# Optimization experiments

Measured on AMD Instinct MI355X. Metric: run time of the kernel, lower is better.

The kernel has to match this reference:

```python
import jax, jax.numpy as jnp
import numpy as np

N_NODES = 50000
N_EDGES = 800000
IN_CH = 16
OUT_CH = 16
HID = 32


def setup_inputs() -> dict:
    key = jax.random.key(0)
    ks = jax.random.split(key, 10)
    features = jax.random.normal(ks[0], (N_NODES, IN_CH), dtype=jnp.float32)
    coords = jax.random.normal(ks[1], (N_NODES, 3), dtype=jnp.float32)
    # edges without self-loops (avoids zero-distance edges)
    row = jax.random.randint(ks[2], (N_EDGES,), 0, N_NODES, dtype=jnp.int32)
    off = jax.random.randint(ks[3], (N_EDGES,), 1, N_NODES, dtype=jnp.int32)
    col = (row + off) % N_NODES
    edge_index = jnp.stack([row, col], axis=0)
    # params (fan-in scaled like torch defaults, roughly)
    w1 = jax.random.normal(ks[4], (1, HID), dtype=jnp.float32)
    b1 = jnp.zeros((HID,), dtype=jnp.float32)
    w2 = jax.random.normal(ks[5], (HID, HID), dtype=jnp.float32) / np.sqrt(HID)
    b2 = jnp.zeros((HID,), dtype=jnp.float32)
    wc = jax.random.normal(ks[6], (HID, IN_CH * OUT_CH), dtype=jnp.float32) / np.sqrt(HID)
    bc = jnp.zeros((IN_CH * OUT_CH,), dtype=jnp.float32)
    return {"features": features, "coords": coords, "edge_index": edge_index,
            "w1": w1, "b1": b1, "w2": w2, "b2": b2, "wc": wc, "bc": bc}


def reference(features, coords, edge_index, w1, b1, w2, b2, wc, bc):
    row, col = edge_index[0], edge_index[1]
    rel_pos = coords[row] - coords[col]                      # [E, 3]
    distances = jnp.sqrt(jnp.sum(rel_pos * rel_pos, axis=-1, keepdims=True))  # [E, 1]
    h = jax.nn.silu(distances @ w1 + b1)                     # [E, H]
    h = jax.nn.silu(h @ w2 + b2)                             # [E, H]
    coeffs = (h @ wc + bc).reshape(-1, OUT_CH, IN_CH)        # [E, out, in]
    # Faithful to torch einsum 'noi,ei->no': the edge axes of coeffs and
    # neighbor_features are DISTINCT labels, so features[col] is summed over
    # all edges, then contracted with each edge's coeff matrix.
    feat_sum = jnp.sum(features[col], axis=0)                # [in]
    messages = jnp.einsum('eoi,i->eo', coeffs, feat_sum)     # [E, out]
    out = jnp.zeros((features.shape[0], OUT_CH), dtype=features.dtype)
    out = out.at[row].add(messages)                          # scatter-add
    return out
```

## Files before the change

kernel.cpp:

```cpp
#include <hip/hip_runtime.h>
#include <hip/hip_bf16.h>

#define IN_CH 16
#define OUT_CH 16
#define HID 32
#define NSLICE 8
#define SDEG 16
#define G_TAB 8192
#define DMAX 16.0f
#define R1_BLOCKS 64
#define TB 256

__device__ __forceinline__ float silu(float x) {
  return x * __frcp_rn(1.f + __expf(-x));
}

__global__ __launch_bounds__(256) void k_pass1(
    const float* __restrict__ feat, const float* __restrict__ coords,
    const int* __restrict__ row, const int* __restrict__ col, int E, int N,
    int* __restrict__ cnt8, float* __restrict__ bucket,
    float* __restrict__ partials) {
  int e = blockIdx.x * blockDim.x + threadIdx.x;
  int lane = threadIdx.x & 63;
  int wave = threadIdx.x >> 6;
  bool act = (e < E);

  float s[IN_CH];
#pragma unroll
  for (int i = 0; i < IN_CH; ++i) s[i] = 0.f;

  int r = 0, pos = SDEG;
  float d = 0.f;
  int slice = blockIdx.x & (NSLICE - 1);

  if (act) {
    r = row[e];
    int c = col[e];

    float rx = coords[r * 3 + 0] - coords[c * 3 + 0];
    float ry = coords[r * 3 + 1] - coords[c * 3 + 1];
    float rz = coords[r * 3 + 2] - coords[c * 3 + 2];
    d = sqrtf(rx * rx + ry * ry + rz * rz);

    pos = atomicAdd(&cnt8[r * NSLICE + slice], 1);

    const float4* fp = reinterpret_cast<const float4*>(feat + (size_t)c * IN_CH);
    float4 a = fp[0], b = fp[1], cc = fp[2], dd = fp[3];
    s[0] = a.x;  s[1] = a.y;  s[2] = a.z;  s[3] = a.w;
    s[4] = b.x;  s[5] = b.y;  s[6] = b.z;  s[7] = b.w;
    s[8] = cc.x; s[9] = cc.y; s[10] = cc.z; s[11] = cc.w;
    s[12] = dd.x; s[13] = dd.y; s[14] = dd.z; s[15] = dd.w;
  }

  __shared__ float red[4][IN_CH];
#pragma unroll
  for (int i = 0; i < IN_CH; ++i) {
    float v = s[i];
#pragma unroll
    for (int off = 32; off > 0; off >>= 1) v += __shfl_down(v, off);
    s[i] = v;
  }
  if (lane == 0) {
#pragma unroll
    for (int i = 0; i < IN_CH; ++i) red[wave][i] = s[i];
  }
  __syncthreads();
  if (threadIdx.x < IN_CH) {
    int i = threadIdx.x;
    partials[(size_t)blockIdx.x * IN_CH + i] =
        red[0][i] + red[1][i] + red[2][i] + red[3][i];
  }

  if (act && pos < SDEG)
    bucket[(size_t)r * (NSLICE * SDEG) + slice * SDEG + pos] = d;
}

__global__ __launch_bounds__(256) void k_reduce1(
    const float* __restrict__ partials, int nrows, float* __restrict__ stage2) {
  __shared__ float red[16][IN_CH];
  int t = threadIdx.x;
  int ch = t & 15, g = t >> 4;
  int stream_id = blockIdx.x * 16 + g;
  int stride = 16 * gridDim.x;
  float a = 0.f;
  for (int rr = stream_id; rr < nrows; rr += stride)
    a += partials[(size_t)rr * IN_CH + ch];
  red[g][ch] = a;
  __syncthreads();
  if (t < IN_CH) {
    float s = 0.f;
#pragma unroll
    for (int g2 = 0; g2 < 16; ++g2) s += red[g2][t];
    stage2[(size_t)blockIdx.x * IN_CH + t] = s;
  }
}

__global__ __launch_bounds__(512) void k_wce(
    const float* __restrict__ rows_in, int nrows,
    const float* __restrict__ wc, const float* __restrict__ bc,
    float* __restrict__ wce, float* __restrict__ bce) {
  __shared__ float seg[32][IN_CH];
  __shared__ float sfs[IN_CH];
  int t = threadIdx.x;
  {
    int ch = t & 15, sg = t >> 4;
    float a = 0.f;
    for (int rr = sg; rr < nrows; rr += 32)
      a += rows_in[(size_t)rr * IN_CH + ch];
    seg[sg][ch] = a;
  }
  __syncthreads();
  if (t < IN_CH) {
    float a = 0.f;
#pragma unroll
    for (int sg = 0; sg < 32; ++sg) a += seg[sg][t];
    sfs[t] = a;
  }
  __syncthreads();

  int k = t >> 4, o = t & 15;
  float acc = 0.f;
#pragma unroll
  for (int i = 0; i < IN_CH; ++i)
    acc += wc[k * (IN_CH * OUT_CH) + o * IN_CH + i] * sfs[i];
  wce[t] = acc;

  if (t < OUT_CH) {
    float a = 0.f;
#pragma unroll
    for (int i = 0; i < IN_CH; ++i) a += bc[t * IN_CH + i] * sfs[i];
    bce[t] = a;
  }
}

__global__ __launch_bounds__(TB) void k_table(
    const float* __restrict__ w1, const float* __restrict__ b1,
    const float* __restrict__ w2, const float* __restrict__ b2,
    const float* __restrict__ wce, const float* __restrict__ bce,
    float* __restrict__ tableP) {
  __shared__ float F[TB][OUT_CH];
  int base = blockIdx.x * (TB - 1);
  int i = base + threadIdx.x;

  float m[OUT_CH];
#pragma unroll
  for (int o = 0; o < OUT_CH; ++o) m[o] = 0.f;

  if (i < G_TAB) {
    float d = (float)i * (DMAX / (float)(G_TAB - 1));

    float h1[HID];
#pragma unroll
    for (int k = 0; k < HID; ++k) h1[k] = silu(d * w1[k] + b1[k]);

    float h2[HID];
#pragma unroll
    for (int k = 0; k < HID; ++k) h2[k] = b2[k];
#pragma unroll
    for (int k = 0; k < HID; ++k) {
      float hk = h1[k];
#pragma unroll
      for (int j = 0; j < HID; ++j) h2[j] += hk * w2[k * HID + j];
    }

#pragma unroll
    for (int o = 0; o < OUT_CH; ++o) m[o] = bce[o];
#pragma unroll
    for (int k = 0; k < HID; ++k) {
      float hk = silu(h2[k]);
#pragma unroll
      for (int o = 0; o < OUT_CH; ++o) m[o] += hk * wce[k * OUT_CH + o];
    }
  }

#pragma unroll
  for (int o = 0; o < OUT_CH; ++o) F[threadIdx.x][o] = m[o];
  __syncthreads();

  const int NV4 = (TB - 1) * OUT_CH * 2 / 4;
  for (int v = threadIdx.x; v < NV4; v += TB) {
    int flat = v * 4;
    int p = flat >> 5;
    int w = flat & 31;
    int c0 = w >> 1;
    int P = base + p;
    if (P < G_TAB - 1) {
      float4 val = make_float4(F[p][c0], F[p + 1][c0],
                               F[p][c0 + 1], F[p + 1][c0 + 1]);
      *reinterpret_cast<float4*>(tableP + ((size_t)P * OUT_CH + c0) * 2) = val;
    }
  }
}

__global__ __launch_bounds__(256) void k_gather_tab(
    const int* __restrict__ cnt8, const float* __restrict__ bucket, int N,
    const float* __restrict__ tableP, float* __restrict__ out) {
  int wave = threadIdx.x >> 6;
  int lane = threadIdx.x & 63;
  int n = blockIdx.x * 4 + wave;
  if (n >= N) return;

  int g = lane >> 4;
  int ch = lane & 15;

  const float2* bp =
      reinterpret_cast<const float2*>(bucket + (size_t)n * (NSLICE * SDEG));
  float2 d2 = bp[lane];

  int c8 = 0;
  if (lane < NSLICE) c8 = cnt8[n * NSLICE + lane];
  int cntA = min(__shfl(c8, g), SDEG);
  int cntB = min(__shfl(c8, g + 4), SDEG);

  int jmax = max(cntA, cntB);
#pragma unroll
  for (int off = 32; off > 0; off >>= 1)
    jmax = max(jmax, __shfl_xor(jmax, off));

  const float inv = (float)(G_TAB - 1) / DMAX;
  float acc = 0.f;
  for (int j = 0; j < jmax; ++j) {
    {
      int slot = g * SDEG + j;
      float dx = __shfl(d2.x, slot >> 1);
      float dy = __shfl(d2.y, slot >> 1);
      float d = (slot & 1) ? dy : dx;
      if (j < cntA) {
        float x = d * inv;
        int i0 = (int)x;
        i0 = min(i0, G_TAB - 2);
        float frac = x - (float)i0;
        float2 f = *reinterpret_cast<const float2*>(
            tableP + ((size_t)i0 * OUT_CH + ch) * 2);
        acc += f.x + frac * (f.y - f.x);
      }
    }
    {
      int slot = (g + 4) * SDEG + j;
      float dx = __shfl(d2.x, slot >> 1);
      float dy = __shfl(d2.y, slot >> 1);
      float d = (slot & 1) ? dy : dx;
      if (j < cntB) {
        float x = d * inv;
        int i0 = (int)x;
        i0 = min(i0, G_TAB - 2);
        float frac = x - (float)i0;
        float2 f = *reinterpret_cast<const float2*>(
            tableP + ((size_t)i0 * OUT_CH + ch) * 2);
        acc += f.x + frac * (f.y - f.x);
      }
    }
  }

  acc += __shfl_xor(acc, 16);
  acc += __shfl_xor(acc, 32);
  if (lane < OUT_CH) out[(size_t)n * OUT_CH + lane] = acc;
}

__global__ __launch_bounds__(256) void k_hist(
    const int* __restrict__ col, int E, int* __restrict__ ccnt) {
  int e = blockIdx.x * blockDim.x + threadIdx.x;
  if (e < E) atomicAdd(&ccnt[col[e]], 1);
}

__global__ __launch_bounds__(256) void k_fs(
    const float* __restrict__ feat, const int* __restrict__ ccnt, int N,
    float* __restrict__ partials) {
  int ch = threadIdx.x & 15;
  int slot = threadIdx.x >> 4;
  int gs = blockIdx.x * 16 + slot;
  int stride = 16 * gridDim.x;
  float a = 0.f;
  for (int n = gs; n < N; n += stride)
    a += (float)ccnt[n] * feat[(size_t)n * IN_CH + ch];
  __shared__ float red[16][IN_CH];
  red[slot][ch] = a;
  __syncthreads();
  if (threadIdx.x < IN_CH) {
    int i = threadIdx.x;
    float s = 0.f;
#pragma unroll
    for (int g = 0; g < 16; ++g) s += red[g][i];
    partials[(size_t)blockIdx.x * IN_CH + i] = s;
  }
}

__global__ __launch_bounds__(256) void k_edges_atomic(
    const float* __restrict__ coords, const int* __restrict__ row,
    const int* __restrict__ col, int E,
    const float* __restrict__ w1, const float* __restrict__ b1,
    const float* __restrict__ w2, const float* __restrict__ b2,
    const float* __restrict__ wce, const float* __restrict__ bce,
    float* __restrict__ out) {
  int e = blockIdx.x * blockDim.x + threadIdx.x;
  if (e >= E) return;
  int r = row[e], c = col[e];
  float rx = coords[r * 3 + 0] - coords[c * 3 + 0];
  float ry = coords[r * 3 + 1] - coords[c * 3 + 1];
  float rz = coords[r * 3 + 2] - coords[c * 3 + 2];
  float d = sqrtf(rx * rx + ry * ry + rz * rz);
  float h1[HID];
#pragma unroll
  for (int k = 0; k < HID; ++k) h1[k] = silu(d * w1[k] + b1[k]);
  float h2[HID];
#pragma unroll
  for (int k = 0; k < HID; ++k) h2[k] = b2[k];
#pragma unroll
  for (int k = 0; k < HID; ++k) {
    float hk = h1[k];
#pragma unroll
    for (int j = 0; j < HID; ++j) h2[j] += hk * w2[k * HID + j];
  }
  float m[OUT_CH];
#pragma unroll
  for (int o = 0; o < OUT_CH; ++o) m[o] = bce[o];
#pragma unroll
  for (int k = 0; k < HID; ++k) {
    float hk = silu(h2[k]);
#pragma unroll
    for (int o = 0; o < OUT_CH; ++o) m[o] += hk * wce[k * OUT_CH + o];
  }
  float* op = out + (size_t)r * OUT_CH;
#pragma unroll
  for (int o = 0; o < OUT_CH; ++o) atomicAdd(op + o, m[o]);
}

extern "C" void kernel_launch(void* const* d_in, const int* in_sizes, int n_in,
                              void* d_out, int out_size, void* d_ws,
                              size_t ws_size, hipStream_t stream) {
  const float* features = (const float*)d_in[0];
  const float* coords   = (const float*)d_in[1];
  const int*   eidx     = (const int*)d_in[2];
  const float* w1       = (const float*)d_in[3];
  const float* b1       = (const float*)d_in[4];
  const float* w2       = (const float*)d_in[5];
  const float* b2       = (const float*)d_in[6];
  const float* wc       = (const float*)d_in[7];
  const float* bc       = (const float*)d_in[8];

  const int E = in_sizes[2] / 2;
  const int N = in_sizes[0] / IN_CH;
  const int* row = eidx;
  const int* col = eidx + E;

  float* out = (float*)d_out;
  const int eb = (E + 255) / 256;

  float* wce      = (float*)d_ws;
  float* bce      = wce + 512;
  float* stage2   = bce + 16;
  float* partials = stage2 + R1_BLOCKS * IN_CH;
  float* tableP   = partials + (size_t)eb * IN_CH;
  int*   cnt8     = (int*)(tableP + (size_t)G_TAB * OUT_CH * 2);
  float* bucket   = (float*)(cnt8 + (size_t)N * NSLICE);

  size_t needed = (512 + 16 + (size_t)R1_BLOCKS * IN_CH + (size_t)eb * IN_CH +
                   (size_t)G_TAB * OUT_CH * 2) * 4 +
                  (size_t)N * NSLICE * 4 + (size_t)N * NSLICE * SDEG * 4;

  if (ws_size >= needed) {
    hipMemsetAsync(cnt8, 0, (size_t)N * NSLICE * sizeof(int), stream);
    k_pass1<<<eb, 256, 0, stream>>>(features, coords, row, col, E, N, cnt8,
                                    bucket, partials);
    k_reduce1<<<R1_BLOCKS, 256, 0, stream>>>(partials, eb, stage2);
    k_wce<<<1, 512, 0, stream>>>(stage2, R1_BLOCKS, wc, bc, wce, bce);
    int tb_grid = (G_TAB - 1 + (TB - 1) - 1) / (TB - 1) + 1;
    k_table<<<tb_grid, TB, 0, stream>>>(w1, b1, w2, b2, wce, bce, tableP);
    int gb = (N + 3) / 4;
    k_gather_tab<<<gb, 256, 0, stream>>>(cnt8, bucket, N, tableP, out);
  } else {
    float* partials_fb = bce + 16;
    int*   ccnt_fb     = (int*)(partials_fb + 64 * IN_CH);
    hipMemsetAsync(ccnt_fb, 0, (size_t)N * sizeof(int), stream);
    hipMemsetAsync(out, 0, (size_t)out_size * sizeof(float), stream);
    k_hist<<<eb, 256, 0, stream>>>(col, E, ccnt_fb);
    k_fs<<<64, 256, 0, stream>>>(features, ccnt_fb, N, partials_fb);
    k_wce<<<1, 512, 0, stream>>>(partials_fb, 64, wc, bc, wce, bce);
    k_edges_atomic<<<eb, 256, 0, stream>>>(coords, row, col, E, w1, b1, w2,
                                           b2, wce, bce, out);
  }
}
```

Before: 100.9 us.

## Compute feature sum via per-column histogram instead of per-edge feature gather

The first pass no longer gathers 64 bytes of features per edge and no longer does a block reduction. Instead it atomically counts column occurrences into sliced counters. A separate kernel then computes the feature sum as a count-weighted sum over nodes, which replaces the partials reduction kernel. The memset is also replaced by a custom zeroing kernel covering both counter arrays. This trades per-edge feature reads and shuffle reductions for an extra atomic per edge and an extra pass over the nodes. In the fallback path the zeroing kernel writes int4 chunks, so it can write up to 3 ints past the N-int counter array.

```diff
diff --git a/kernel.cpp b/kernel.cpp
--- a/kernel.cpp
+++ b/kernel.cpp
@@ -8,90 +8,62 @@
 #define SDEG 16
 #define G_TAB 8192
 #define DMAX 16.0f
-#define R1_BLOCKS 64
 #define TB 256
 
 __device__ __forceinline__ float silu(float x) {
   return x * __frcp_rn(1.f + __expf(-x));
 }
 
+__global__ __launch_bounds__(256) void k_zero(int4* __restrict__ p, int n4) {
+  int i = blockIdx.x * blockDim.x + threadIdx.x;
+  if (i < n4) p[i] = make_int4(0, 0, 0, 0);
+}
+
 __global__ __launch_bounds__(256) void k_pass1(
-    const float* __restrict__ feat, const float* __restrict__ coords,
-    const int* __restrict__ row, const int* __restrict__ col, int E, int N,
-    int* __restrict__ cnt8, float* __restrict__ bucket,
+    const float* __restrict__ coords, const int* __restrict__ row,
+    const int* __restrict__ col, int E,
+    int* __restrict__ cnt8, int* __restrict__ ccnt8,
+    float* __restrict__ bucket) {
+  int e = blockIdx.x * blockDim.x + threadIdx.x;
+  if (e >= E) return;
+  int slice = blockIdx.x & (NSLICE - 1);
+  int r = row[e], c = col[e];
+
+  atomicAdd(&ccnt8[c * NSLICE + slice], 1);
+
+  float rx = coords[r * 3 + 0] - coords[c * 3 + 0];
+  float ry = coords[r * 3 + 1] - coords[c * 3 + 1];
+  float rz = coords[r * 3 + 2] - coords[c * 3 + 2];
+  float d = sqrtf(rx * rx + ry * ry + rz * rz);
+
+  int pos = atomicAdd(&cnt8[r * NSLICE + slice], 1);
+  if (pos < SDEG)
+    bucket[(size_t)r * (NSLICE * SDEG) + slice * SDEG + pos] = d;
+}
+
+__global__ __launch_bounds__(256) void k_fs8(
+    const float* __restrict__ feat, const int* __restrict__ ccnt8, int N,
     float* __restrict__ partials) {
-  int e = blockIdx.x * blockDim.x + threadIdx.x;
-  int lane = threadIdx.x & 63;
-  int wave = threadIdx.x >> 6;
-  bool act = (e < E);
-
-  float s[IN_CH];
-#pragma unroll
-  for (int i = 0; i < IN_CH; ++i) s[i] = 0.f;
-
-  int r = 0, pos = SDEG;
-  float d = 0.f;
-  int slice = blockIdx.x & (NSLICE - 1);
-
-  if (act) {
-    r = row[e];
-    int c = col[e];
-
-    float rx = coords[r * 3 + 0] - coords[c * 3 + 0];
-    float ry = coords[r * 3 + 1] - coords[c * 3 + 1];
-    float rz = coords[r * 3 + 2] - coords[c * 3 + 2];
-    d = sqrtf(rx * rx + ry * ry + rz * rz);
-
-    pos = atomicAdd(&cnt8[r * NSLICE + slice], 1);
-
-    const float4* fp = reinterpret_cast<const float4*>(feat + (size_t)c * IN_CH);
-    float4 a = fp[0], b = fp[1], cc = fp[2], dd = fp[3];
-    s[0] = a.x;  s[1] = a.y;  s[2] = a.z;  s[3] = a.w;
-    s[4] = b.x;  s[5] = b.y;  s[6] = b.z;  s[7] = b.w;
-    s[8] = cc.x; s[9] = cc.y; s[10] = cc.z; s[11] = cc.w;
-    s[12] = dd.x; s[13] = dd.y; s[14] = dd.z; s[15] = dd.w;
-  }
-
-  __shared__ float red[4][IN_CH];
-#pragma unroll
-  for (int i = 0; i < IN_CH; ++i) {
-    float v = s[i];
-#pragma unroll
-    for (int off = 32; off > 0; off >>= 1) v += __shfl_down(v, off);
-    s[i] = v;
-  }
-  if (lane == 0) {
-#pragma unroll
-    for (int i = 0; i < IN_CH; ++i) red[wave][i] = s[i];
-  }
+  int ch = threadIdx.x & 15;
+  int slot = threadIdx.x >> 4;
+  int gs = blockIdx.x * 16 + slot;
+  int stride = 16 * gridDim.x;
+  float a = 0.f;
+  for (int n = gs; n < N; n += stride) {
+    const int4* cp = reinterpret_cast<const int4*>(ccnt8 + (size_t)n * NSLICE);
+    int4 c0 = cp[0], c1 = cp[1];
+    float w = (float)(c0.x + c0.y + c0.z + c0.w + c1.x + c1.y + c1.z + c1.w);
+    a += w * feat[(size_t)n * IN_CH + ch];
+  }
+  __shared__ float red[16][IN_CH];
+  red[slot][ch] = a;
   __syncthreads();
   if (threadIdx.x < IN_CH) {
     int i = threadIdx.x;
-    partials[(size_t)blockIdx.x * IN_CH + i] =
-        red[0][i] + red[1][i] + red[2][i] + red[3][i];
-  }
-
-  if (act && pos < SDEG)
-    bucket[(size_t)r * (NSLICE * SDEG) + slice * SDEG + pos] = d;
-}
-
-__global__ __launch_bounds__(256) void k_reduce1(
-    const float* __restrict__ partials, int nrows, float* __restrict__ stage2) {
-  __shared__ float red[16][IN_CH];
-  int t = threadIdx.x;
-  int ch = t & 15, g = t >> 4;
-  int stream_id = blockIdx.x * 16 + g;
-  int stride = 16 * gridDim.x;
-  float a = 0.f;
-  for (int rr = stream_id; rr < nrows; rr += stride)
-    a += partials[(size_t)rr * IN_CH + ch];
-  red[g][ch] = a;
-  __syncthreads();
-  if (t < IN_CH) {
     float s = 0.f;
 #pragma unroll
-    for (int g2 = 0; g2 < 16; ++g2) s += red[g2][t];
-    stage2[(size_t)blockIdx.x * IN_CH + t] = s;
+    for (int g = 0; g < 16; ++g) s += red[g][i];
+    partials[(size_t)blockIdx.x * IN_CH + i] = s;
   }
 }
 
@@ -348,22 +320,21 @@
 
   float* wce      = (float*)d_ws;
   float* bce      = wce + 512;
-  float* stage2   = bce + 16;
-  float* partials = stage2 + R1_BLOCKS * IN_CH;
-  float* tableP   = partials + (size_t)eb * IN_CH;
+  float* partials = bce + 16;
+  float* tableP   = partials + 64 * IN_CH;
   int*   cnt8     = (int*)(tableP + (size_t)G_TAB * OUT_CH * 2);
-  float* bucket   = (float*)(cnt8 + (size_t)N * NSLICE);
-
-  size_t needed = (512 + 16 + (size_t)R1_BLOCKS * IN_CH + (size_t)eb * IN_CH +
-                   (size_t)G_TAB * OUT_CH * 2) * 4 +
-                  (size_t)N * NSLICE * 4 + (size_t)N * NSLICE * SDEG * 4;
+  int*   ccnt8    = cnt8 + (size_t)N * NSLICE;
+  float* bucket   = (float*)(ccnt8 + (size_t)N * NSLICE);
+
+  size_t needed = (512 + 16 + 64 * IN_CH + (size_t)G_TAB * OUT_CH * 2) * 4 +
+                  (size_t)N * NSLICE * 8 + (size_t)N * NSLICE * SDEG * 4;
 
   if (ws_size >= needed) {
-    hipMemsetAsync(cnt8, 0, (size_t)N * NSLICE * sizeof(int), stream);
-    k_pass1<<<eb, 256, 0, stream>>>(features, coords, row, col, E, N, cnt8,
-                                    bucket, partials);
-    k_reduce1<<<R1_BLOCKS, 256, 0, stream>>>(partials, eb, stage2);
-    k_wce<<<1, 512, 0, stream>>>(stage2, R1_BLOCKS, wc, bc, wce, bce);
+    int n4 = (int)(((size_t)N * NSLICE * 2) / 4);
+    k_zero<<<(n4 + 255) / 256, 256, 0, stream>>>((int4*)cnt8, n4);
+    k_pass1<<<eb, 256, 0, stream>>>(coords, row, col, E, cnt8, ccnt8, bucket);
+    k_fs8<<<64, 256, 0, stream>>>(features, ccnt8, N, partials);
+    k_wce<<<1, 512, 0, stream>>>(partials, 64, wc, bc, wce, bce);
     int tb_grid = (G_TAB - 1 + (TB - 1) - 1) / (TB - 1) + 1;
     k_table<<<tb_grid, TB, 0, stream>>>(w1, b1, w2, b2, wce, bce, tableP);
     int gb = (N + 3) / 4;
@@ -371,7 +342,8 @@
   } else {
     float* partials_fb = bce + 16;
     int*   ccnt_fb     = (int*)(partials_fb + 64 * IN_CH);
-    hipMemsetAsync(ccnt_fb, 0, (size_t)N * sizeof(int), stream);
+    int nz4 = (N + 3) / 4;
+    k_zero<<<(nz4 + 255) / 256, 256, 0, stream>>>((int4*)ccnt_fb, nz4);
     hipMemsetAsync(out, 0, (size_t)out_size * sizeof(float), stream);
     k_hist<<<eb, 256, 0, stream>>>(col, E, ccnt_fb);
     k_fs<<<64, 256, 0, stream>>>(features, ccnt_fb, N, partials_fb);
```

Result: slower. 145.5 us (+44.1%).
